# Performance work log

Measured on AMD Instinct MI355X. Metric: run time of the kernel, lower is better.

The kernel has to match this reference:

```python
import jax, jax.numpy as jnp
import numpy as np
from jax.scipy.special import gammaln, logsumexp

S, K, O, H = 64, 16, 32, 30   # state_dim, act_dim, obs_dim, horizon
T, N = 200, 512               # seq len, batch
EPS = 1e-6
LOG2PI = float(np.log(2.0 * np.pi))
NUM_PARAMS = S * O * 2 + K * S * S + S + S + 1


def setup_inputs() -> dict:
    key = jax.random.key(0)
    k1, k2, k3 = jax.random.split(key, 3)
    o = jax.random.normal(k1, (T, N, O), dtype=jnp.float32)
    a = jax.random.randint(k2, (T, N), 0, K)
    theta = jax.random.normal(k3, (N, NUM_PARAMS), dtype=jnp.float32)
    return {"o": o, "a": a, "theta": theta}


def _transform_params(theta):
    sizes = [S * O * 2, K * S * S, S, S, 1]
    idx = np.cumsum(sizes)[:-1]
    tA, tB, tC, tD, ttau = jnp.split(theta, idx, axis=-1)
    A_mean, A_lv = jnp.split(tA, 2, axis=-1)
    A_mean = A_mean.reshape(-1, S, O)
    A_std = jax.nn.softplus(A_lv.reshape(-1, S, O)) + EPS  # rectify
    B = jax.nn.softmax(tB.reshape(-1, K, S, S), axis=-1)
    C = jax.nn.softmax(tC.reshape(-1, 1, S), axis=-1)
    D = jax.nn.softmax(tD.reshape(-1, S), axis=-1)
    tau = jax.nn.sigmoid(ttau) * (2.0 * H) + 1.0  # [N,1]
    return A_mean, A_std, B, C, D, tau


def reference(o, a, theta):
    A_mean, A_std, B, C, D, tau = _transform_params(theta)

    # --- negative expected free energy reward: r[n,k,i] ---
    ent = jnp.sum(0.5 + 0.5 * LOG2PI + jnp.log(A_std), axis=-1)          # Normal entropy, [N,S]
    kl = jnp.sum(B * (jnp.log(B + EPS) - jnp.log(C[:, None] + EPS)), -1)  # KL(B || C), [N,K,S]
    eh = jnp.einsum('nkij,nj->nki', B, ent)
    r = -kl - eh

    # --- finite-horizon value iteration: q [H,N,K,S] ---
    def vi_step(qt, _):
        v = logsumexp(qt, axis=-2)                    # [N,S]
        qn = r + jnp.einsum('nkij,nj->nki', B, v)
        return qn, qn
    _, q_rest = jax.lax.scan(vi_step, r, None, length=H - 1)
    q = jnp.concatenate([r[None], q_rest], axis=0)

    # --- truncated poisson horizon weights: pdf [N,H] ---
    hh = jnp.arange(H, dtype=jnp.float32)
    logp_h = hh[None, :] * jnp.log(tau) - tau - gammaln(hh + 1.0)[None, :]
    pdf = jnp.exp(logp_h)
    pdf = pdf / jnp.sum(pdf, axis=-1, keepdims=True)

    batch_idx = jnp.arange(N)

    def time_step(b, inp):
        o_t, a_t = inp
        # policy from current belief
        qb = jnp.einsum('ni,hnki->hnk', b, q)
        pi_h = jax.nn.softmax(qb, axis=-1)
        pi_t = jnp.einsum('hnk,nh->nk', pi_h, pdf)
        # belief update
        B_a = B[batch_idx, a_t]                       # [N,S,S]
        s = jnp.einsum('nij,ni->nj', B_a, b)
        logp_s = jnp.log(s + EPS)
        lp = -0.5 * ((o_t[:, None, :] - A_mean) / A_std) ** 2 \
             - jnp.log(A_std) - 0.5 * LOG2PI          # [N,S,O]
        joint = logp_s + jnp.sum(lp, axis=-1)         # [N,S]
        b_next = jax.nn.softmax(joint, axis=-1)
        logp_o = logsumexp(joint, axis=-1)
        return b_next, (pi_t, b, logp_o)

    _, (pi, b_seq, logp_o) = jax.lax.scan(time_step, D, (o, a))
    return pi, b_seq, logp_o
```

## Files before the change

### kernel.cpp

```cpp
#include <hip/hip_runtime.h>
#include <hip/hip_bf16.h>
#include <math.h>

#define SDIM 64
#define KDIM 16
#define ODIM 32
#define HDIM 30
#define TDIM 200
#define NDIM 512
#define NP 69761
#define EPSV 1e-6f
#define LOG2PIF 1.8378770664093453f

__device__ __forceinline__ float softplusf(float x) {
    return (x > 0.f) ? x + log1pf(expf(-x)) : log1pf(expf(x));
}
__device__ __forceinline__ float wave_max64(float v) {
#pragma unroll
    for (int off = 32; off; off >>= 1) v = fmaxf(v, __shfl_xor(v, off, 64));
    return v;
}
__device__ __forceinline__ float wave_sum64(float v) {
#pragma unroll
    for (int off = 32; off; off >>= 1) v += __shfl_xor(v, off, 64);
// ... 7 lines not shown
    const float* __restrict__ theta, float* __restrict__ invstd,
    float* __restrict__ c0, float* __restrict__ ent,
    float* __restrict__ logC, float* __restrict__ Dws,
    float* __restrict__ pdfws)
{
    __shared__ float ls[SDIM * 33];
    const int n = blockIdx.x, tid = threadIdx.x;
    const float* thn = theta + (size_t)n * NP;

    for (int idx = tid; idx < SDIM * ODIM; idx += 256) {
        float x = thn[2048 + idx];
        float sp = softplusf(x) + EPSV;
        invstd[(size_t)n * SDIM * ODIM + idx] = 1.f / sp;
        int s = idx >> 5, oo = idx & 31;
        ls[s * 33 + oo] = logf(sp);
    }
    __syncthreads();

    const int wave = tid >> 6, lane = tid & 63;
    if (wave == 0) {
        float sum = 0.f;
#pragma unroll
        for (int oo = 0; oo < ODIM; ++oo) sum += ls[lane * 33 + oo];
        c0[n * SDIM + lane]  = -sum - 16.f * LOG2PIF;
        ent[n * SDIM + lane] =  sum + 32.f * (0.5f + 0.5f * LOG2PIF);
    } else if (wave == 1) {
        float x = thn[69632 + lane];
        float m = wave_max64(x);
        float e = expf(x - m);
        float ssum = wave_sum64(e);
        logC[n * SDIM + lane] = logf(e / ssum + EPSV);
    } else if (wave == 2) {
        float x = thn[69696 + lane];
        float m = wave_max64(x);
        float e = expf(x - m);
        float ssum = wave_sum64(e);
        Dws[n * SDIM + lane] = e / ssum;
    } else {
        float tt = thn[69760];
        float tau = 60.f / (1.f + expf(-tt)) + 1.f;
        float p = 0.f;
        if (lane < HDIM)
            p = expf((float)lane * logf(tau) - tau - lgammaf((float)lane + 1.f));
        float ssum = wave_sum64(p);
        if (lane < HDIM) pdfws[n * HDIM + lane] = p / ssum;
    }
}

__global__ __launch_bounds__(256) void row_stats_kernel(
    const float* __restrict__ theta, const float* __restrict__ logC,
    const float* __restrict__ ent, float* __restrict__ lse,
    float* __restrict__ rws, __hip_bfloat16* __restrict__ bn)
{
    const int gw = blockIdx.x * 4 + (threadIdx.x >> 6);
    const int lane = threadIdx.x & 63;
    const int n = gw >> 10, rl = gw & 1023;
    float x = theta[(size_t)n * NP + 4096 + (size_t)rl * 64 + lane];
    float m = wave_max64(x);
    float e = expf(x - m);
    float ssum = wave_sum64(e);
    float Bj = e / ssum;
    if (bn) {
        const int k = rl >> 6, i = rl & 63;
        __hip_bfloat16 h = __float2bfloat16(Bj);
        unsigned short bits;
        __builtin_memcpy(&bits, &h, 2);
        ((unsigned short*)bn)[(size_t)n * KDIM * SDIM * SDIM
            + (size_t)k * 4096 + (size_t)(i >> 1) * 128 + lane * 2 + (i & 1)] = bits;
    }
    float contrib = Bj * (logf(Bj + EPSV) - logC[n * SDIM + lane] + ent[n * SDIM + lane]);
    contrib = wave_sum64(contrib);
    if (lane == 0) {
        lse[gw] = m + logf(ssum);
        rws[gw] = -contrib;
    }
}

#define BS4(T_, U_) do {                                                       \
    const int cur_ = (T_) & 1, nxt_ = cur_ ^ 1;                                \
    if (wave == 3) out_b[((size_t)(T_) * NDIM + n) * SDIM + lane] = bval;      \
    {      \
        float a0_ = 0.f, a1_ = 0.f, a2_ = 0.f, a3_ = 0.f;                      \
        _Pragma("unroll")                                                      \
        for (int j_ = 0; j_ < 4; ++j_) {                                       \
            a0_ += er[4 * j_ + 0] * __shfl(bval, rbase + 4 * j_ + 0, 64);      \
            a1_ += er[4 * j_ + 1] * __shfl(bval, rbase + 4 * j_ + 1, 64);      \
            a2_ += er[4 * j_ + 2] * __shfl(bval, rbase + 4 * j_ + 2, 64);      \
            a3_ += er[4 * j_ + 3] * __shfl(bval, rbase + 4 * j_ + 3, 64);      \
        }                                                                      \
        part_s[cur_][wave][lane] = (a0_ + a1_) + (a2_ + a3_);                  \
    }                                                                          \
    if ((T_) + 1 < TDIM) {                             \
        const float* om_ = &o_s[((T_) + 1) * ODIM + ob];                       \
        float zz_ = 0.f;                                                       \
        _Pragma("unroll")                                                      \
        for (int j_ = 0; j_ < 8; ++j_) {                                       \
            float z_ = (om_[j_] - mean_r[j_]) * istd_r[j_];                    \
            zz_ += z_ * z_;                                                    \
        }                                                                      \
        z2p_s[nxt_][wave][lane] = zz_;                                         \
    }                                                                          \
    _Pragma("unroll")                             \
    for (int m_ = 0; m_ < 8; ++m_) {                                           \
        er[2 * m_]     = __uint_as_float(U_[m_] << 16);                        \
        er[2 * m_ + 1] = __uint_as_float(U_[m_] & 0xffff0000u);                \
    }                                                                          \
    {                                                 \
        const int tl_ = ((T_) + 3 < TDIM) ? (T_) + 3 : TDIM - 1;               \
        const uint* up_ = bnn32 + (size_t)a_s[tl_] * 2048 + (rbase >> 1) * 64 + lane; \
        _Pragma("unroll")                                                      \
        for (int m_ = 0; m_ < 8; ++m_) U_[m_] = up_[m_ * 64];                  \
    }                                                                          \
    bar_lds();                                            \
    {            \
        float sv_ = part_s[cur_][0][lane] + part_s[cur_][1][lane]              \
                  + part_s[cur_][2][lane] + part_s[cur_][3][lane];             \
        float u_ = (sv_ + EPSV) * ecz_cur;                                     \
        float S_ = wave_sum64(u_);                                             \
        if (wave == 0 && lane == 0)                                            \
            out_lp[(size_t)(T_) * NDIM + n] = cm_cur + __logf(S_);             \
        bval = u_ / S_;                                                        \
        float z2n_ = z2p_s[nxt_][0][lane] + z2p_s[nxt_][1][lane]               \
                   + z2p_s[nxt_][2][lane] + z2p_s[nxt_][3][lane];              \
        float cn_ = c0_r - 0.5f * z2n_;                                        \
        cm_cur = wave_max64(cn_);                                              \
        ecz_cur = __expf(cn_ - cm_cur);                                        \
    }                                                                          \
} while (0)

__global__ __launch_bounds__(256) void belief4_kernel(
    const float* __restrict__ o, const int* __restrict__ a,
    const float* __restrict__ theta, const __hip_bfloat16* __restrict__ bn,
    const float* __restrict__ invstd, const float* __restrict__ c0g,
    const float* __restrict__ Dws,
    float* __restrict__ out_b, float* __restrict__ out_lp)
{
    __shared__ float o_s[TDIM * ODIM];
    __shared__ int   a_s[TDIM];
    __shared__ float mean_s[SDIM * 33];
    __shared__ float istd_s[SDIM * 33];
    __shared__ float c0_sh[SDIM];
    __shared__ float part_s[2][4][68];
    __shared__ float z2p_s[2][4][SDIM];

    const int n = blockIdx.x, tid = threadIdx.x;
    const int wave = tid >> 6, lane = tid & 63;
    const int rbase = wave * 16, ob = wave * 8;
    const float* thn = theta + (size_t)n * NP;
    const uint* bnn32 = (const uint*)(bn + (size_t)n * KDIM * SDIM * SDIM);

    for (int idx = tid; idx < TDIM * ODIM; idx += 256)
        o_s[idx] = o[((size_t)(idx >> 5) * NDIM + n) * ODIM + (idx & 31)];
    if (tid < TDIM) a_s[tid] = a[tid * NDIM + n];
    for (int idx = tid; idx < SDIM * ODIM; idx += 256) {
        int s = idx >> 5, oo = idx & 31;
        mean_s[s * 33 + oo] = thn[idx];
        istd_s[s * 33 + oo] = invstd[(size_t)n * SDIM * ODIM + idx];
    }
    if (tid < SDIM) c0_sh[tid] = c0g[n * SDIM + tid];
    __syncthreads();

    const float c0_r = c0_sh[lane];
    float bval = Dws[n * SDIM + lane];
    float mean_r[8], istd_r[8];
#pragma unroll
    for (int j = 0; j < 8; ++j) {
        mean_r[j] = mean_s[lane * 33 + ob + j];
        istd_r[j] = istd_s[lane * 33 + ob + j];
    }

    float er[16];
    uint u0[8], u1[8];
    {
        const uint* p0 = bnn32 + (size_t)a_s[0] * 2048 + (rbase >> 1) * 64 + lane;
#pragma unroll
        for (int m = 0; m < 8; ++m) u0[m] = p0[m * 64];
#pragma unroll
        for (int m = 0; m < 8; ++m) {
            er[2 * m]     = __uint_as_float(u0[m] << 16);
            er[2 * m + 1] = __uint_as_float(u0[m] & 0xffff0000u);
        }
        const uint* p1 = bnn32 + (size_t)a_s[1] * 2048 + (rbase >> 1) * 64 + lane;
#pragma unroll
        for (int m = 0; m < 8; ++m) u0[m] = p1[m * 64];
        const uint* p2 = bnn32 + (size_t)a_s[2] * 2048 + (rbase >> 1) * 64 + lane;
#pragma unroll
        for (int m = 0; m < 8; ++m) u1[m] = p2[m * 64];
    }
    {
        const float* om = &o_s[ob];
        float zz = 0.f;
#pragma unroll
        for (int j = 0; j < 8; ++j) {
            float z = (om[j] - mean_r[j]) * istd_r[j];
            zz += z * z;
        }
        z2p_s[0][wave][lane] = zz;
    }
    __syncthreads();
    float ecz_cur, cm_cur;
    {
        float z2 = z2p_s[0][0][lane] + z2p_s[0][1][lane]
                 + z2p_s[0][2][lane] + z2p_s[0][3][lane];
        float c = c0_r - 0.5f * z2;
        cm_cur = wave_max64(c);
        ecz_cur = __expf(c - cm_cur);
    }

#pragma unroll 1
    for (int t = 0; t < TDIM; t += 2) {
        BS4(t, u0);
        BS4(t + 1, u1);
    }
}

#define Z2PART(TT_, BUF_) do {                                                 \
    const int ob_ = (wave - 1) * 8;                                            \
    const float* om_ = &o_s[(TT_) * ODIM + ob_];                               \
    float zz_ = 0.f;                                                           \
    _Pragma("unroll")                                                          \
    for (int j_ = 0; j_ < 8; ++j_) {                                           \
        float z_ = (om_[j_] - mean_s[lane * 33 + ob_ + j_])                    \
                 * istd_s[lane * 33 + ob_ + j_];                               \
        zz_ += z_ * z_;                                                        \
    }                                                                          \
    z2p_s[BUF_][wave - 1][lane] = zz_;                                         \
} while (0)

#define BSTEP(T_, RAW_) do {                                                   \
    const int cur_ = (T_) & 1, nxt_ = cur_ ^ 1;                                \
    if (wave >= 1) {                                                           \
        float acc_ = 0.f;                                                      \
        _Pragma("unroll")                                                      \
        for (int ii = 0; ii < 10; ++ii)                                        \
            if (ii < nrow) acc_ += er[ii] * b_s[cur_][rbase + ii];             \
        part_s[wave - 1][lane] = acc_;                                         \
        if (wave == 6) out_b[((size_t)(T_) * NDIM + n) * SDIM + lane] = b_s[cur_][lane]; \
    }                                                                          \
    bar_lds();                                                                 \
    if (wave == 0) {                                                           \
        float sv_ = part_s[0][lane] + part_s[1][lane] + part_s[2][lane]        \
                  + part_s[3][lane] + part_s[4][lane] + part_s[5][lane]        \
                  + part_s[6][lane];                                           \
        float z2_ = z2p_s[cur_][0][lane] + z2p_s[cur_][1][lane]                \
                  + z2p_s[cur_][2][lane] + z2p_s[cur_][3][lane];               \
        float joint_ = __logf(sv_ + EPSV) + c0_s[lane] - 0.5f * z2_;           \
        float m_ = wave_max64(joint_);                                         \
        float e_ = __expf(joint_ - m_);                                        \
        float ss_ = wave_sum64(e_);                                            \
        b_s[nxt_][lane] = e_ / ss_;                                            \
        if (lane == 0) out_lp[(size_t)(T_) * NDIM + n] = m_ + __logf(ss_);     \
    } else {                                                                   \
        if ((T_) + 1 < TDIM) {                                                 \
            const int an_ = a_s[(T_) + 1];                                     \
            const float* ln_ = lseA + an_ * SDIM;                              \
            _Pragma("unroll")                                                  \
            for (int ii = 0; ii < 10; ++ii)                                    \
                if (ii < nrow) er[ii] = __expf(RAW_[ii] - ln_[rbase + ii]);    \
            if (wave <= 4) Z2PART((T_) + 1, nxt_);                             \
        }                                                                      \
        const int tl_ = ((T_) + 3 < TDIM) ? (T_) + 3 : TDIM - 1;               \
        const int a3_ = a_s[tl_];                                              \
        const float* X3_ = Xn + (size_t)a3_ * SDIM * SDIM;                     \
        _Pragma("unroll")                                                      \
        for (int ii = 0; ii < 10; ++ii)                                        \
// ... 17 lines not shown
    __shared__ float c0_s[SDIM];
    __shared__ float b_s[2][SDIM];
    __shared__ float part_s[7][68];
    __shared__ float z2p_s[2][4][SDIM];

    const int n = blockIdx.x, tid = threadIdx.x;
    const int wave = tid >> 6, lane = tid & 63;
    const float* thn = theta + (size_t)n * NP;
    const float* Xn  = thn + 4096;

    for (int idx = tid; idx < TDIM * ODIM; idx += 512)
        o_s[idx] = o[((size_t)(idx >> 5) * NDIM + n) * ODIM + (idx & 31)];
    if (tid < TDIM) a_s[tid] = a[tid * NDIM + n];
    for (int idx = tid; idx < SDIM * ODIM; idx += 512) {
        int s = idx >> 5, oo = idx & 31;
        mean_s[s * 33 + oo] = thn[idx];
        istd_s[s * 33 + oo] = invstd[(size_t)n * SDIM * ODIM + idx];
    }
    for (int idx = tid; idx < KDIM * SDIM; idx += 512)
        lseA[idx] = lse[(size_t)n * KDIM * SDIM + idx];
    if (tid < SDIM) { c0_s[tid] = c0g[n * SDIM + tid]; b_s[0][tid] = Dws[n * SDIM + tid]; }
    __syncthreads();

    const int rbase = (wave >= 1) ? (wave - 1) * 10 : 0;
    const int nrow  = (wave >= 1) ? ((SDIM - rbase) < 10 ? (SDIM - rbase) : 10) : 0;

    float er[10], raw0[10], raw1[10];
    if (wave >= 1) {
        const int a0 = a_s[0];
        const float* X0 = Xn + (size_t)a0 * SDIM * SDIM;
        const float* l0 = lseA + a0 * SDIM;
#pragma unroll
        for (int ii = 0; ii < 10; ++ii)
            if (ii < nrow) er[ii] = __expf(X0[(size_t)(rbase + ii) * SDIM + lane] - l0[rbase + ii]);
        const int a1 = a_s[1];
        const float* X1 = Xn + (size_t)a1 * SDIM * SDIM;
#pragma unroll
        for (int ii = 0; ii < 10; ++ii)
            if (ii < nrow) raw0[ii] = X1[(size_t)(rbase + ii) * SDIM + lane];
        const int a2 = a_s[2];
        const float* X2 = Xn + (size_t)a2 * SDIM * SDIM;
#pragma unroll
        for (int ii = 0; ii < 10; ++ii)
            if (ii < nrow) raw1[ii] = X2[(size_t)(rbase + ii) * SDIM + lane];
        if (wave <= 4) Z2PART(0, 0);
    }
    __syncthreads();

#pragma unroll 1
    for (int t = 0; t < TDIM; t += 2) {
        BSTEP(t, raw0);
        BSTEP(t + 1, raw1);
    }
}

__global__ __launch_bounds__(512) void vi_kernel(
    const float* __restrict__ theta, const float* __restrict__ lse,
    const float* __restrict__ rws, float* __restrict__ q_ws)
{
    __shared__ float q_lds[KDIM * 68];
    __shared__ __align__(16) float v_lds[68];
    const int n = blockIdx.x, tid = threadIdx.x;
    const float* Xn = theta + (size_t)n * NP + 4096;

    const float l0  = lse[(size_t)n * 1024 + tid];
    const float l1  = lse[(size_t)n * 1024 + 512 + tid];
    const float rr0 = rws[(size_t)n * 1024 + tid];
    const float rr1 = rws[(size_t)n * 1024 + 512 + tid];

    float4 er0[16], er1[16];
    {
        const float* X0 = Xn + (size_t)tid * 64;
        const float* X1 = Xn + (size_t)(512 + tid) * 64;
#pragma unroll
        for (int j = 0; j < 16; ++j) {
            float4 x = *(const float4*)(X0 + j * 4);
            er0[j] = make_float4(__expf(x.x - l0), __expf(x.y - l0),
                                 __expf(x.z - l0), __expf(x.w - l0));
            float4 y = *(const float4*)(X1 + j * 4);
            er1[j] = make_float4(__expf(y.x - l1), __expf(y.y - l1),
                                 __expf(y.z - l1), __expf(y.w - l1));
        }
    }

    float qr0 = rr0, qr1 = rr1;
    float* qw = q_ws + (size_t)n * HDIM * 1024;
    const int kq0 = tid >> 6, iq = tid & 63;
    qw[tid] = qr0;
    qw[512 + tid] = qr1;
    q_lds[kq0 * 68 + iq] = qr0;
    q_lds[(8 + kq0) * 68 + iq] = qr1;
    __syncthreads();

#pragma unroll 1
    for (int h = 1; h < HDIM; ++h) {
        if (tid < 64) {
            float m = -1e30f;
#pragma unroll
            for (int k = 0; k < KDIM; ++k) m = fmaxf(m, q_lds[k * 68 + tid]);
            float s = 0.f;
#pragma unroll
            for (int k = 0; k < KDIM; ++k) s += __expf(q_lds[k * 68 + tid] - m);
            v_lds[tid] = m + __logf(s);
        }
        bar_lds();
        float a0x = 0.f, a0y = 0.f, a0z = 0.f, a0w = 0.f;
        float a1x = 0.f, a1y = 0.f, a1z = 0.f, a1w = 0.f;
#pragma unroll
        for (int jq = 0; jq < 16; ++jq) {
            const float4 v4 = *(const float4*)&v_lds[jq * 4];
            a0x += er0[jq].x * v4.x; a0y += er0[jq].y * v4.y;
            a0z += er0[jq].z * v4.z; a0w += er0[jq].w * v4.w;
            a1x += er1[jq].x * v4.x; a1y += er1[jq].y * v4.y;
            a1z += er1[jq].z * v4.z; a1w += er1[jq].w * v4.w;
        }
        qr0 = rr0 + ((a0x + a0y) + (a0z + a0w));
        qr1 = rr1 + ((a1x + a1y) + (a1z + a1w));
        qw[(size_t)h * 1024 + tid] = qr0;
        qw[(size_t)h * 1024 + 512 + tid] = qr1;
        q_lds[kq0 * 68 + iq] = qr0;
        q_lds[(8 + kq0) * 68 + iq] = qr1;
        bar_lds();
    }
}

__global__ __launch_bounds__(512, 1) void policy_bc_kernel(
    const float* __restrict__ q_ws, const float* __restrict__ out_b_g,
    const float* __restrict__ pdfg, float* __restrict__ out_pi)
{
    __shared__ __align__(16) float b_all[TDIM * SDIM];
    __shared__ float part[2][8][8][17];
    __shared__ float pdf_s[32];

    const int n = blockIdx.x, tid = threadIdx.x;
    const int w = tid >> 6, lane = tid & 63;
    const int hl = lane >> 4, kk = lane & 15;
    const int hown = w * 4 + hl;
    const float* qn = q_ws + (size_t)n * HDIM * 1024;

    for (int idx = tid; idx < TDIM * 16; idx += 512) {
        const int t = idx >> 4, jq = idx & 15;
        *(float4*)&b_all[t * SDIM + jq * 4] =
            *(const float4*)&out_b_g[((size_t)t * NDIM + n) * SDIM + jq * 4];
    }
    if (tid < 32) pdf_s[tid] = (tid < HDIM) ? pdfg[n * HDIM + tid] : 0.f;

    float4 qrow[16];
    if (hown < HDIM) {
#pragma unroll
        for (int jq = 0; jq < 16; ++jq)
            qrow[jq] = *(const float4*)&qn[(size_t)hown * 1024 + kk * 64 + jq * 4];
    } else {
#pragma unroll
        for (int jq = 0; jq < 16; ++jq)
            qrow[jq] = make_float4(0.f, 0.f, 0.f, 0.f);
    }
    __syncthreads();
    const float pdfh = pdf_s[hown];

#define PVAL(T_, OUTV_) do {                                                   \
    const float* br_ = &b_all[(T_) * SDIM];                                    \
    float ax_ = 0.f, ay_ = 0.f, az_ = 0.f, aw_ = 0.f;                          \
    _Pragma("unroll")                                                          \
    for (int jq_ = 0; jq_ < 16; ++jq_) {                                       \
        const float4 b4_ = *(const float4*)&br_[jq_ * 4];                      \
        ax_ += qrow[jq_].x * b4_.x; ay_ += qrow[jq_].y * b4_.y;                \
        az_ += qrow[jq_].z * b4_.z; aw_ += qrow[jq_].w * b4_.w;                \
    }                                                                          \
    float acc_ = (ax_ + ay_) + (az_ + aw_);                                    \
    float m_ = acc_;                                                           \
    m_ = fmaxf(m_, __shfl_xor(m_, 1, 64));                                     \
    m_ = fmaxf(m_, __shfl_xor(m_, 2, 64));                                     \
    m_ = fmaxf(m_, __shfl_xor(m_, 4, 64));                                     \
    m_ = fmaxf(m_, __shfl_xor(m_, 8, 64));                                     \
    float e_ = __expf(acc_ - m_);                                              \
    float S_ = e_;                                                             \
    S_ += __shfl_xor(S_, 1, 64);                                               \
    S_ += __shfl_xor(S_, 2, 64);                                               \
    S_ += __shfl_xor(S_, 4, 64);                                               \
    S_ += __shfl_xor(S_, 8, 64);                                               \
    float v_ = pdfh * e_ / S_;                                                 \
    v_ += __shfl_xor(v_, 16, 64);                                              \
    v_ += __shfl_xor(v_, 32, 64);                                              \
    OUTV_ = v_;                                                                \
} while (0)

#pragma unroll 1
    for (int t0 = 0; t0 < TDIM; t0 += 8) {
        const int buf = (t0 >> 3) & 1;
        float v0, v1, v2, v3, v4, v5, v6, v7;
        PVAL(t0 + 0, v0); PVAL(t0 + 1, v1); PVAL(t0 + 2, v2); PVAL(t0 + 3, v3);
        PVAL(t0 + 4, v4); PVAL(t0 + 5, v5); PVAL(t0 + 6, v6); PVAL(t0 + 7, v7);
        if (lane < 16) {
            part[buf][0][w][lane] = v0; part[buf][1][w][lane] = v1;
            part[buf][2][w][lane] = v2; part[buf][3][w][lane] = v3;
            part[buf][4][w][lane] = v4; part[buf][5][w][lane] = v5;
            part[buf][6][w][lane] = v6; part[buf][7][w][lane] = v7;
        }
        bar_lds();
        if (lane < 16) {
            float s8 = 0.f;
#pragma unroll
            for (int ww = 0; ww < 8; ++ww) s8 += part[buf][w][ww][lane];
            out_pi[((size_t)(t0 + w) * NDIM + n) * KDIM + lane] = s8;
        }
    }
#undef PVAL
}

__global__ __launch_bounds__(512) void vi_policy_kernel(
    const float* __restrict__ theta, const float* __restrict__ lse,
    const float* __restrict__ rws, const float* __restrict__ pdfg,
    const float* __restrict__ out_b_g, float* __restrict__ out_pi)
{
    __shared__ __align__(16) float q_s[HDIM * KDIM * 68];
    __shared__ float r_s[KDIM * SDIM];
    __shared__ float lse_s[KDIM * SDIM];
    __shared__ __align__(16) float v_s[SDIM];
    __shared__ __align__(16) float b_lds[64 * 68];
    __shared__ float pdf_s[32];

    const int n = blockIdx.x, tid = threadIdx.x;
    const int wave = tid >> 6, lane = tid & 63;
    const int sub = lane & 15, rq = lane >> 4;
    const float* Xn = theta + (size_t)n * NP + 4096;

    for (int idx = tid; idx < KDIM * SDIM; idx += 512) {
        r_s[idx]   = rws[(size_t)n * KDIM * SDIM + idx];
        lse_s[idx] = lse[(size_t)n * KDIM * SDIM + idx];
    }
    if (tid < HDIM) pdf_s[tid] = pdfg[n * HDIM + tid];
    __syncthreads();

    for (int idx = tid; idx < KDIM * SDIM; idx += 512)
        q_s[(idx >> 6) * 68 + (idx & 63)] = r_s[idx];

    float4 breg[32];
#pragma unroll
    for (int it = 0; it < 32; ++it) {
        const int row = it * 32 + wave * 4 + rq;
        const float* xr = Xn + (size_t)row * SDIM + sub * 4;
        const float l = lse_s[row];
        breg[it] = make_float4(__expf(xr[0] - l), __expf(xr[1] - l),
                               __expf(xr[2] - l), __expf(xr[3] - l));
    }
    bar_lds();

#pragma unroll 1
    for (int h = 1; h < HDIM; ++h) {
        if (tid < SDIM) {
            const int base = (h - 1) * KDIM;
            float m = -1e30f;
#pragma unroll
            for (int k = 0; k < KDIM; ++k) m = fmaxf(m, q_s[(base + k) * 68 + tid]);
            float ssum = 0.f;
#pragma unroll
            for (int k = 0; k < KDIM; ++k) ssum += __expf(q_s[(base + k) * 68 + tid] - m);
            v_s[tid] = m + __logf(ssum);
        }
        bar_lds();
// ... 53 lines not shown
            mA = fmaxf(mA, __shfl_xor(mA, 2, 64));
            mA = fmaxf(mA, __shfl_xor(mA, 4, 64));
            mA = fmaxf(mA, __shfl_xor(mA, 8, 64));
            mB = fmaxf(mB, __shfl_xor(mB, 1, 64));
            mB = fmaxf(mB, __shfl_xor(mB, 2, 64));
            mB = fmaxf(mB, __shfl_xor(mB, 4, 64));
            mB = fmaxf(mB, __shfl_xor(mB, 8, 64));
            float eA = __expf(aA - mA), eB = __expf(aB - mB);
            float SA = eA, SB = eB;
            SA += __shfl_xor(SA, 1, 64);
            SA += __shfl_xor(SA, 2, 64);
            SA += __shfl_xor(SA, 4, 64);
            SA += __shfl_xor(SA, 8, 64);
            SB += __shfl_xor(SB, 1, 64);
            SB += __shfl_xor(SB, 2, 64);
            SB += __shfl_xor(SB, 4, 64);
            SB += __shfl_xor(SB, 8, 64);
            const float ph = pdf_s[h];
            pikA += ph * eA / SA;
            pikB += ph * eB / SB;
        }
        if (vA) out_pi[(((size_t)(t0 + tc)) * NDIM + n) * KDIM + kk] = pikA;
        if (vB) out_pi[(((size_t)(t0 + 32 + tc)) * NDIM + n) * KDIM + kk] = pikB;
        bar_lds();
    }
}

extern "C" void kernel_launch(void* const* d_in, const int* in_sizes, int n_in,
                              void* d_out, int out_size, void* d_ws, size_t ws_size,
                              hipStream_t stream) {
    (void)in_sizes; (void)n_in; (void)out_size;
    const float* o     = (const float*)d_in[0];
    const int*   a     = (const int*)d_in[1];
    const float* theta = (const float*)d_in[2];
    float* out = (float*)d_out;
    float* ws  = (float*)d_ws;

    float* lse    = ws;
    float* rws    = lse    + (size_t)NDIM * KDIM * SDIM;
    float* invstd = rws    + (size_t)NDIM * KDIM * SDIM;
    float* c0     = invstd + (size_t)NDIM * SDIM * ODIM;
    float* ent    = c0     + (size_t)NDIM * SDIM;
    float* logC   = ent    + (size_t)NDIM * SDIM;
    float* Dws    = logC   + (size_t)NDIM * SDIM;
    float* pdfws  = Dws    + (size_t)NDIM * SDIM;
    float* q_ws   = pdfws  + (size_t)NDIM * HDIM;
    __hip_bfloat16* bn = (__hip_bfloat16*)(q_ws + (size_t)NDIM * HDIM * KDIM * SDIM);

    const size_t f_base = (size_t)NDIM * KDIM * SDIM * 2
                        + (size_t)NDIM * SDIM * ODIM
                        + (size_t)NDIM * SDIM * 4
                        + (size_t)NDIM * HDIM;
    const size_t f_q  = (size_t)NDIM * HDIM * KDIM * SDIM;
    const size_t need2 = (f_base + f_q) * 4;
    const size_t need1 = need2 + (size_t)NDIM * KDIM * SDIM * SDIM * 2;

    float* out_pi = out;
    float* out_b  = out + (size_t)TDIM * NDIM * KDIM;
    float* out_lp = out + (size_t)TDIM * NDIM * KDIM + (size_t)TDIM * NDIM * SDIM;

    transform_kernel<<<NDIM, 256, 0, stream>>>(theta, invstd, c0, ent, logC, Dws, pdfws);

    if (ws_size >= need1) {
        row_stats_kernel<<<(NDIM * KDIM * SDIM) / 4, 256, 0, stream>>>(
            theta, logC, ent, lse, rws, bn);
        belief4_kernel<<<NDIM, 256, 0, stream>>>(
            o, a, theta, bn, invstd, c0, Dws, out_b, out_lp);
        vi_kernel<<<NDIM, 512, 0, stream>>>(theta, lse, rws, q_ws);
        policy_bc_kernel<<<NDIM, 512, 0, stream>>>(q_ws, out_b, pdfws, out_pi);
    } else if (ws_size >= need2) {
        row_stats_kernel<<<(NDIM * KDIM * SDIM) / 4, 256, 0, stream>>>(
            theta, logC, ent, lse, rws, (__hip_bfloat16*)nullptr);
        belief_kernel<<<NDIM, 512, 0, stream>>>(
            o, a, theta, lse, invstd, c0, Dws, out_b, out_lp);
        vi_kernel<<<NDIM, 512, 0, stream>>>(theta, lse, rws, q_ws);
        policy_bc_kernel<<<NDIM, 512, 0, stream>>>(q_ws, out_b, pdfws, out_pi);
    } else {
        row_stats_kernel<<<(NDIM * KDIM * SDIM) / 4, 256, 0, stream>>>(
            theta, logC, ent, lse, rws, (__hip_bfloat16*)nullptr);
        belief_kernel<<<NDIM, 512, 0, stream>>>(
            o, a, theta, lse, invstd, c0, Dws, out_b, out_lp);
        vi_policy_kernel<<<NDIM, 512, 0, stream>>>(theta, lse, rws, pdfws, out_b, out_pi);
    }
}
```

Measured before the change: 643.4 us.

## Halve policy kernel threads with two horizons per lane and bf16 beliefs in LDS

The policy kernel now runs 256 threads, and each lane owns two horizon rows of q in registers instead of one, so every belief read from LDS is reused twice. The per-sequence belief buffer is stored in LDS as bf16 and unpacked with shifts and masks. This halves LDS use and read traffic, which could let more blocks fit per CU. The cost is lower precision in the belief-q dot product and about twice the register pressure per thread.

```diff
diff --git a/kernel.cpp b/kernel.cpp
--- a/kernel.cpp
+++ b/kernel.cpp
@@ -437,62 +437,92 @@
     }
 }
 
-__global__ __launch_bounds__(512, 1) void policy_bc_kernel(
+__global__ __launch_bounds__(256, 1) void policy_p2_kernel(
     const float* __restrict__ q_ws, const float* __restrict__ out_b_g,
     const float* __restrict__ pdfg, float* __restrict__ out_pi)
 {
-    __shared__ __align__(16) float b_all[TDIM * SDIM];
-    __shared__ float part[2][8][8][17];
+    __shared__ __align__(16) unsigned short b16[TDIM * SDIM];
+    __shared__ float part[2][8][4][17];
     __shared__ float pdf_s[32];
 
     const int n = blockIdx.x, tid = threadIdx.x;
     const int w = tid >> 6, lane = tid & 63;
     const int hl = lane >> 4, kk = lane & 15;
-    const int hown = w * 4 + hl;
+    const int h0 = w * 8 + hl, h1 = h0 + 4;
     const float* qn = q_ws + (size_t)n * HDIM * 1024;
 
-    for (int idx = tid; idx < TDIM * 16; idx += 512) {
-        const int t = idx >> 4, jq = idx & 15;
-        *(float4*)&b_all[t * SDIM + jq * 4] =
-            *(const float4*)&out_b_g[((size_t)t * NDIM + n) * SDIM + jq * 4];
+    for (int idx = tid; idx < TDIM * SDIM; idx += 256) {
+        float bv = out_b_g[((size_t)(idx >> 6) * NDIM + n) * SDIM + (idx & 63)];
+        __hip_bfloat16 hb = __float2bfloat16(bv);
+        unsigned short bits; __builtin_memcpy(&bits, &hb, 2);
+        b16[idx] = bits;
     }
     if (tid < 32) pdf_s[tid] = (tid < HDIM) ? pdfg[n * HDIM + tid] : 0.f;
 
-    float4 qrow[16];
-    if (hown < HDIM) {
+    float4 q0[16], q1[16];
+    if (h0 < HDIM) {
 #pragma unroll
         for (int jq = 0; jq < 16; ++jq)
-            qrow[jq] = *(const float4*)&qn[(size_t)hown * 1024 + kk * 64 + jq * 4];
+            q0[jq] = *(const float4*)&qn[(size_t)h0 * 1024 + kk * 64 + jq * 4];
     } else {
 #pragma unroll
+        for (int jq = 0; jq < 16; ++jq) q0[jq] = make_float4(0.f, 0.f, 0.f, 0.f);
+    }
+    if (h1 < HDIM) {
+#pragma unroll
         for (int jq = 0; jq < 16; ++jq)
-            qrow[jq] = make_float4(0.f, 0.f, 0.f, 0.f);
+            q1[jq] = *(const float4*)&qn[(size_t)h1 * 1024 + kk * 64 + jq * 4];
+    } else {
+#pragma unroll
+        for (int jq = 0; jq < 16; ++jq) q1[jq] = make_float4(0.f, 0.f, 0.f, 0.f);
     }
     __syncthreads();
-    const float pdfh = pdf_s[hown];
-
-#define PVAL(T_, OUTV_) do {                                                   \
-    const float* br_ = &b_all[(T_) * SDIM];                                    \
-    float ax_ = 0.f, ay_ = 0.f, az_ = 0.f, aw_ = 0.f;                          \
+    const float pdf0 = pdf_s[h0], pdf1 = pdf_s[h1];
+
+#define PVAL2(T_, OUTV_) do {                                                  \
+    const uint4* bp_ = (const uint4*)&b16[(T_) * SDIM];                        \
+    float a0x_ = 0.f, a0y_ = 0.f, a0z_ = 0.f, a0w_ = 0.f;                      \
+    float a1x_ = 0.f, a1y_ = 0.f, a1z_ = 0.f, a1w_ = 0.f;                      \
     _Pragma("unroll")                                                          \
-    for (int jq_ = 0; jq_ < 16; ++jq_) {                                       \
-        const float4 b4_ = *(const float4*)&br_[jq_ * 4];                      \
-        ax_ += qrow[jq_].x * b4_.x; ay_ += qrow[jq_].y * b4_.y;                \
-        az_ += qrow[jq_].z * b4_.z; aw_ += qrow[jq_].w * b4_.w;                \
-    }                                                                          \
-    float acc_ = (ax_ + ay_) + (az_ + aw_);                                    \
-    float m_ = acc_;                                                           \
-    m_ = fmaxf(m_, __shfl_xor(m_, 1, 64));                                     \
-    m_ = fmaxf(m_, __shfl_xor(m_, 2, 64));                                     \
-    m_ = fmaxf(m_, __shfl_xor(m_, 4, 64));                                     \
-    m_ = fmaxf(m_, __shfl_xor(m_, 8, 64));                                     \
-    float e_ = __expf(acc_ - m_);                                              \
-    float S_ = e_;                                                             \
-    S_ += __shfl_xor(S_, 1, 64);                                               \
-    S_ += __shfl_xor(S_, 2, 64);                                               \
-    S_ += __shfl_xor(S_, 4, 64);                                               \
-    S_ += __shfl_xor(S_, 8, 64);                                               \
-    float v_ = pdfh * e_ / S_;                                                 \
+    for (int r_ = 0; r_ < 8; ++r_) {                                           \
+        const uint4 u_ = bp_[r_];                                              \
+        const float b0_ = __uint_as_float(u_.x << 16);                         \
+        const float b1_ = __uint_as_float(u_.x & 0xffff0000u);                 \
+        const float b2_ = __uint_as_float(u_.y << 16);                         \
+        const float b3_ = __uint_as_float(u_.y & 0xffff0000u);                 \
+        const float b4_ = __uint_as_float(u_.z << 16);                         \
+        const float b5_ = __uint_as_float(u_.z & 0xffff0000u);                 \
+        const float b6_ = __uint_as_float(u_.w << 16);                         \
+        const float b7_ = __uint_as_float(u_.w & 0xffff0000u);                 \
+        const float4 qa0_ = q0[2 * r_], qb0_ = q0[2 * r_ + 1];                 \
+        const float4 qa1_ = q1[2 * r_], qb1_ = q1[2 * r_ + 1];                 \
+        a0x_ += qa0_.x * b0_; a0y_ += qa0_.y * b1_;                            \
+        a0z_ += qa0_.z * b2_; a0w_ += qa0_.w * b3_;                            \
+        a0x_ += qb0_.x * b4_; a0y_ += qb0_.y * b5_;                            \
+        a0z_ += qb0_.z * b6_; a0w_ += qb0_.w * b7_;                            \
+        a1x_ += qa1_.x * b0_; a1y_ += qa1_.y * b1_;                            \
+        a1z_ += qa1_.z * b2_; a1w_ += qa1_.w * b3_;                            \
+        a1x_ += qb1_.x * b4_; a1y_ += qb1_.y * b5_;                            \
+        a1z_ += qb1_.z * b6_; a1w_ += qb1_.w * b7_;                            \
+    }                                                                          \
+    float acc0_ = (a0x_ + a0y_) + (a0z_ + a0w_);                               \
+    float acc1_ = (a1x_ + a1y_) + (a1z_ + a1w_);                               \
+    float m0_ = acc0_, m1_ = acc1_;                                            \
+    m0_ = fmaxf(m0_, __shfl_xor(m0_, 1, 64));                                  \
+    m1_ = fmaxf(m1_, __shfl_xor(m1_, 1, 64));                                  \
+    m0_ = fmaxf(m0_, __shfl_xor(m0_, 2, 64));                                  \
+    m1_ = fmaxf(m1_, __shfl_xor(m1_, 2, 64));                                  \
+    m0_ = fmaxf(m0_, __shfl_xor(m0_, 4, 64));                                  \
+    m1_ = fmaxf(m1_, __shfl_xor(m1_, 4, 64));                                  \
+    m0_ = fmaxf(m0_, __shfl_xor(m0_, 8, 64));                                  \
+    m1_ = fmaxf(m1_, __shfl_xor(m1_, 8, 64));                                  \
+    float e0_ = __expf(acc0_ - m0_), e1_ = __expf(acc1_ - m1_);                \
+    float S0_ = e0_, S1_ = e1_;                                                \
+    S0_ += __shfl_xor(S0_, 1, 64);  S1_ += __shfl_xor(S1_, 1, 64);             \
+    S0_ += __shfl_xor(S0_, 2, 64);  S1_ += __shfl_xor(S1_, 2, 64);             \
+    S0_ += __shfl_xor(S0_, 4, 64);  S1_ += __shfl_xor(S1_, 4, 64);             \
+    S0_ += __shfl_xor(S0_, 8, 64);  S1_ += __shfl_xor(S1_, 8, 64);             \
+    float v_ = pdf0 * e0_ / S0_ + pdf1 * e1_ / S1_;                            \
     v_ += __shfl_xor(v_, 16, 64);                                              \
     v_ += __shfl_xor(v_, 32, 64);                                              \
     OUTV_ = v_;                                                                \
@@ -502,8 +532,8 @@
     for (int t0 = 0; t0 < TDIM; t0 += 8) {
         const int buf = (t0 >> 3) & 1;
         float v0, v1, v2, v3, v4, v5, v6, v7;
-        PVAL(t0 + 0, v0); PVAL(t0 + 1, v1); PVAL(t0 + 2, v2); PVAL(t0 + 3, v3);
-        PVAL(t0 + 4, v4); PVAL(t0 + 5, v5); PVAL(t0 + 6, v6); PVAL(t0 + 7, v7);
+        PVAL2(t0 + 0, v0); PVAL2(t0 + 1, v1); PVAL2(t0 + 2, v2); PVAL2(t0 + 3, v3);
+        PVAL2(t0 + 4, v4); PVAL2(t0 + 5, v5); PVAL2(t0 + 6, v6); PVAL2(t0 + 7, v7);
         if (lane < 16) {
             part[buf][0][w][lane] = v0; part[buf][1][w][lane] = v1;
             part[buf][2][w][lane] = v2; part[buf][3][w][lane] = v3;
@@ -512,13 +542,15 @@
         }
         bar_lds();
         if (lane < 16) {
-            float s8 = 0.f;
-#pragma unroll
-            for (int ww = 0; ww < 8; ++ww) s8 += part[buf][w][ww][lane];
-            out_pi[((size_t)(t0 + w) * NDIM + n) * KDIM + lane] = s8;
-        }
-    }
-#undef PVAL
+            float sA = part[buf][w][0][lane] + part[buf][w][1][lane]
+                     + part[buf][w][2][lane] + part[buf][w][3][lane];
+            out_pi[((size_t)(t0 + w) * NDIM + n) * KDIM + lane] = sA;
+            float sB = part[buf][w + 4][0][lane] + part[buf][w + 4][1][lane]
+                     + part[buf][w + 4][2][lane] + part[buf][w + 4][3][lane];
+            out_pi[((size_t)(t0 + 4 + w) * NDIM + n) * KDIM + lane] = sB;
+        }
+    }
+#undef PVAL2
 }
 
 __global__ __launch_bounds__(512) void vi_policy_kernel(
@@ -693,14 +725,14 @@
         belief4_kernel<<<NDIM, 256, 0, stream>>>(
             o, a, theta, bn, invstd, c0, Dws, out_b, out_lp);
         vi_kernel<<<NDIM, 512, 0, stream>>>(theta, lse, rws, q_ws);
-        policy_bc_kernel<<<NDIM, 512, 0, stream>>>(q_ws, out_b, pdfws, out_pi);
+        policy_p2_kernel<<<NDIM, 256, 0, stream>>>(q_ws, out_b, pdfws, out_pi);
     } else if (ws_size >= need2) {
         row_stats_kernel<<<(NDIM * KDIM * SDIM) / 4, 256, 0, stream>>>(
             theta, logC, ent, lse, rws, (__hip_bfloat16*)nullptr);
         belief_kernel<<<NDIM, 512, 0, stream>>>(
             o, a, theta, lse, invstd, c0, Dws, out_b, out_lp);
         vi_kernel<<<NDIM, 512, 0, stream>>>(theta, lse, rws, q_ws);
-        policy_bc_kernel<<<NDIM, 512, 0, stream>>>(q_ws, out_b, pdfws, out_pi);
+        policy_p2_kernel<<<NDIM, 256, 0, stream>>>(q_ws, out_b, pdfws, out_pi);
     } else {
         row_stats_kernel<<<(NDIM * KDIM * SDIM) / 4, 256, 0, stream>>>(
             theta, logC, ent, lse, rws, (__hip_bfloat16*)nullptr);
```

Result: slower. 661.0 us (+2.7%).

## Fuse policy computation into belief recurrence and batch row-stats rows per wave

Applied to the files above, without the earlier changes.

The separate policy kernel is removed. Its per-timestep q·b softmax and pdf-weighted mix now run inside the belief recurrence, using q rows held in registers and the current belief shared through LDS. This drops the re-read of the belief sequence from global memory and one kernel launch, but it lengthens every serial belief step and raises register pressure (launch bounds 256,2). The row-stats kernel now handles 16 rows per wave with fewer blocks, and vi_kernel must run before the fused kernel.

```diff
diff --git a/kernel.cpp b/kernel.cpp
--- a/kernel.cpp
+++ b/kernel.cpp
@@ -83,34 +83,114 @@
     const float* __restrict__ ent, float* __restrict__ lse,
     float* __restrict__ rws, __hip_bfloat16* __restrict__ bn)
 {
-    const int gw = blockIdx.x * 4 + (threadIdx.x >> 6);
     const int lane = threadIdx.x & 63;
-    const int n = gw >> 10, rl = gw & 1023;
-    float x = theta[(size_t)n * NP + 4096 + (size_t)rl * 64 + lane];
-    float m = wave_max64(x);
-    float e = expf(x - m);
-    float ssum = wave_sum64(e);
-    float Bj = e / ssum;
-    if (bn) {
-        const int k = rl >> 6, i = rl & 63;
-        __hip_bfloat16 h = __float2bfloat16(Bj);
-        unsigned short bits;
-        __builtin_memcpy(&bits, &h, 2);
-        ((unsigned short*)bn)[(size_t)n * KDIM * SDIM * SDIM
-            + (size_t)k * 4096 + (size_t)(i >> 1) * 128 + lane * 2 + (i & 1)] = bits;
-    }
-    float contrib = Bj * (logf(Bj + EPSV) - logC[n * SDIM + lane] + ent[n * SDIM + lane]);
-    contrib = wave_sum64(contrib);
-    if (lane == 0) {
-        lse[gw] = m + logf(ssum);
-        rws[gw] = -contrib;
-    }
-}
-
-#define BS4(T_, U_) do {                                                       \
+    const int base_row = (blockIdx.x * 4 + (threadIdx.x >> 6)) * 16;
+    const int n = base_row >> 10;
+    const float lC = logC[n * SDIM + lane];
+    const float en = ent[n * SDIM + lane];
+    const float* thb = theta + (size_t)n * NP + 4096;
+    unsigned short* bns = bn ? (unsigned short*)bn + (size_t)n * KDIM * SDIM * SDIM : nullptr;
+
+#pragma unroll 1
+    for (int r = 0; r < 16; ++r) {
+        const int row = base_row + r;
+        const int rl = row & 1023;
+        float x = thb[(size_t)rl * 64 + lane];
+        float m = wave_max64(x);
+        float e = expf(x - m);
+        float ssum = wave_sum64(e);
+        float Bj = e / ssum;
+        if (bns) {
+            const int k = rl >> 6, i = rl & 63;
+            __hip_bfloat16 h = __float2bfloat16(Bj);
+            unsigned short bits;
+            __builtin_memcpy(&bits, &h, 2);
+            bns[(size_t)k * 4096 + (size_t)(i >> 1) * 128 + lane * 2 + (i & 1)] = bits;
+        }
+        float contrib = Bj * (logf(Bj + EPSV) - lC + en);
+        contrib = wave_sum64(contrib);
+        if (lane == 0) {
+            lse[row] = m + logf(ssum);
+            rws[row] = -contrib;
+        }
+    }
+}
+
+__global__ __launch_bounds__(512) void vi_kernel(
+    const float* __restrict__ theta, const float* __restrict__ lse,
+    const float* __restrict__ rws, float* __restrict__ q_ws)
+{
+    __shared__ float q_lds[KDIM * 68];
+    __shared__ __align__(16) float v_lds[68];
+    const int n = blockIdx.x, tid = threadIdx.x;
+    const float* Xn = theta + (size_t)n * NP + 4096;
+
+    const float l0  = lse[(size_t)n * 1024 + tid];
+    const float l1  = lse[(size_t)n * 1024 + 512 + tid];
+    const float rr0 = rws[(size_t)n * 1024 + tid];
+    const float rr1 = rws[(size_t)n * 1024 + 512 + tid];
+
+    float4 er0[16], er1[16];
+    {
+        const float* X0 = Xn + (size_t)tid * 64;
+        const float* X1 = Xn + (size_t)(512 + tid) * 64;
+#pragma unroll
+        for (int j = 0; j < 16; ++j) {
+            float4 x = *(const float4*)(X0 + j * 4);
+            er0[j] = make_float4(__expf(x.x - l0), __expf(x.y - l0),
+                                 __expf(x.z - l0), __expf(x.w - l0));
+            float4 y = *(const float4*)(X1 + j * 4);
+            er1[j] = make_float4(__expf(y.x - l1), __expf(y.y - l1),
+                                 __expf(y.z - l1), __expf(y.w - l1));
+        }
+    }
+
+    float qr0 = rr0, qr1 = rr1;
+    float* qw = q_ws + (size_t)n * HDIM * 1024;
+    const int kq0 = tid >> 6, iq = tid & 63;
+    qw[tid] = qr0;
+    qw[512 + tid] = qr1;
+    q_lds[kq0 * 68 + iq] = qr0;
+    q_lds[(8 + kq0) * 68 + iq] = qr1;
+    __syncthreads();
+
+#pragma unroll 1
+    for (int h = 1; h < HDIM; ++h) {
+        if (tid < 64) {
+            float m = -1e30f;
+#pragma unroll
+            for (int k = 0; k < KDIM; ++k) m = fmaxf(m, q_lds[k * 68 + tid]);
+            float s = 0.f;
+#pragma unroll
+            for (int k = 0; k < KDIM; ++k) s += __expf(q_lds[k * 68 + tid] - m);
+            v_lds[tid] = m + __logf(s);
+        }
+        bar_lds();
+        float a0x = 0.f, a0y = 0.f, a0z = 0.f, a0w = 0.f;
+        float a1x = 0.f, a1y = 0.f, a1z = 0.f, a1w = 0.f;
+#pragma unroll
+        for (int jq = 0; jq < 16; ++jq) {
+            const float4 v4 = *(const float4*)&v_lds[jq * 4];
+            a0x += er0[jq].x * v4.x; a0y += er0[jq].y * v4.y;
+            a0z += er0[jq].z * v4.z; a0w += er0[jq].w * v4.w;
+            a1x += er1[jq].x * v4.x; a1y += er1[jq].y * v4.y;
+            a1z += er1[jq].z * v4.z; a1w += er1[jq].w * v4.w;
+        }
+        qr0 = rr0 + ((a0x + a0y) + (a0z + a0w));
+        qr1 = rr1 + ((a1x + a1y) + (a1z + a1w));
+        qw[(size_t)h * 1024 + tid] = qr0;
+        qw[(size_t)h * 1024 + 512 + tid] = qr1;
+        q_lds[kq0 * 68 + iq] = qr0;
+        q_lds[(8 + kq0) * 68 + iq] = qr1;
+        bar_lds();
+    }
+}
+
+#define BSP(T_, U_) do {                                                       \
     const int cur_ = (T_) & 1, nxt_ = cur_ ^ 1;                                \
     if (wave == 3) out_b[((size_t)(T_) * NDIM + n) * SDIM + lane] = bval;      \
-    {      \
+    if (wave == 1) b2_s[cur_][lane] = bval;                                    \
+    {                                       \
         float a0_ = 0.f, a1_ = 0.f, a2_ = 0.f, a3_ = 0.f;                      \
         _Pragma("unroll")                                                      \
         for (int j_ = 0; j_ < 4; ++j_) {                                       \
@@ -143,7 +223,7 @@
         for (int m_ = 0; m_ < 8; ++m_) U_[m_] = up_[m_ * 64];                  \
     }                                                                          \
     bar_lds();                                            \
-    {            \
+    {                   \
         float sv_ = part_s[cur_][0][lane] + part_s[cur_][1][lane]              \
                   + part_s[cur_][2][lane] + part_s[cur_][3][lane];             \
         float u_ = (sv_ + EPSV) * ecz_cur;                                     \
@@ -157,14 +237,54 @@
         cm_cur = wave_max64(cn_);                                              \
         ecz_cur = __expf(cn_ - cm_cur);                                        \
     }                                                                          \
+    {                     \
+        float aAx_ = 0.f, aAy_ = 0.f, aAz_ = 0.f, aAw_ = 0.f;                  \
+        float aBx_ = 0.f, aBy_ = 0.f, aBz_ = 0.f, aBw_ = 0.f;                  \
+        _Pragma("unroll")                                                      \
+        for (int jq_ = 0; jq_ < 16; ++jq_) {                                   \
+            const float4 b4_ = *(const float4*)&b2_s[cur_][jq_ * 4];           \
+            aAx_ += qA[jq_].x * b4_.x; aAy_ += qA[jq_].y * b4_.y;              \
+            aAz_ += qA[jq_].z * b4_.z; aAw_ += qA[jq_].w * b4_.w;              \
+            aBx_ += qB[jq_].x * b4_.x; aBy_ += qB[jq_].y * b4_.y;              \
+            aBz_ += qB[jq_].z * b4_.z; aBw_ += qB[jq_].w * b4_.w;              \
+        }                                                                      \
+        float aA_ = (aAx_ + aAy_) + (aAz_ + aAw_);                             \
+        float aB_ = (aBx_ + aBy_) + (aBz_ + aBw_);                             \
+        float mA_ = aA_, mB_ = aB_;                                            \
+        mA_ = fmaxf(mA_, __shfl_xor(mA_, 1, 64));                              \
+        mB_ = fmaxf(mB_, __shfl_xor(mB_, 1, 64));                              \
+        mA_ = fmaxf(mA_, __shfl_xor(mA_, 2, 64));                              \
+        mB_ = fmaxf(mB_, __shfl_xor(mB_, 2, 64));                              \
+        mA_ = fmaxf(mA_, __shfl_xor(mA_, 4, 64));                              \
+        mB_ = fmaxf(mB_, __shfl_xor(mB_, 4, 64));                              \
+        mA_ = fmaxf(mA_, __shfl_xor(mA_, 8, 64));                              \
+        mB_ = fmaxf(mB_, __shfl_xor(mB_, 8, 64));                              \
+        float eA_ = __expf(aA_ - mA_), eB_ = __expf(aB_ - mB_);                \
+        float SA_ = eA_, SB_ = eB_;                                            \
+        SA_ += __shfl_xor(SA_, 1, 64);  SB_ += __shfl_xor(SB_, 1, 64);         \
+        SA_ += __shfl_xor(SA_, 2, 64);  SB_ += __shfl_xor(SB_, 2, 64);         \
+        SA_ += __shfl_xor(SA_, 4, 64);  SB_ += __shfl_xor(SB_, 4, 64);         \
+        SA_ += __shfl_xor(SA_, 8, 64);  SB_ += __shfl_xor(SB_, 8, 64);         \
+        float val_ = pdfA * eA_ / SA_ + pdfB * eB_ / SB_;                      \
+        val_ += __shfl_xor(val_, 16, 64);                                      \
+        val_ += __shfl_xor(val_, 32, 64);                                      \
+        if (lane < 16) p2_s[cur_][wave][lane] = val_;                          \
+        if ((T_) > 0 && wave == 3 && lane < 16) {                              \
+            float s4_ = p2_s[nxt_][0][lane] + p2_s[nxt_][1][lane]              \
+                      + p2_s[nxt_][2][lane] + p2_s[nxt_][3][lane];             \
+            out_pi[((size_t)((T_) - 1) * NDIM + n) * KDIM + lane] = s4_;       \
+        }                                                                      \
+    }                                                                          \
 } while (0)
 
-__global__ __launch_bounds__(256) void belief4_kernel(
+__global__ __launch_bounds__(256, 2) void bp_kernel(
     const float* __restrict__ o, const int* __restrict__ a,
     const float* __restrict__ theta, const __hip_bfloat16* __restrict__ bn,
     const float* __restrict__ invstd, const float* __restrict__ c0g,
-    const float* __restrict__ Dws,
-    float* __restrict__ out_b, float* __restrict__ out_lp)
+    const float* __restrict__ Dws, const float* __restrict__ pdfg,
+    const float* __restrict__ q_ws,
+    float* __restrict__ out_pi, float* __restrict__ out_b,
+    float* __restrict__ out_lp)
 {
     __shared__ float o_s[TDIM * ODIM];
     __shared__ int   a_s[TDIM];
@@ -173,6 +293,8 @@
     __shared__ float c0_sh[SDIM];
     __shared__ float part_s[2][4][68];
     __shared__ float z2p_s[2][4][SDIM];
+    __shared__ __align__(16) float b2_s[2][SDIM];
+    __shared__ float p2_s[2][4][17];
 
     const int n = blockIdx.x, tid = threadIdx.x;
     const int wave = tid >> 6, lane = tid & 63;
@@ -189,6 +311,23 @@
         istd_s[s * 33 + oo] = invstd[(size_t)n * SDIM * ODIM + idx];
     }
     if (tid < SDIM) c0_sh[tid] = c0g[n * SDIM + tid];
+
+    const int hA = tid >> 4, kA = tid & 15, hB = hA + 16;
+    const float* qnp = q_ws + (size_t)n * HDIM * 1024;
+    float4 qA[16], qB[16];
+#pragma unroll
+    for (int jq = 0; jq < 16; ++jq)
+        qA[jq] = *(const float4*)&qnp[(size_t)hA * 1024 + kA * 64 + jq * 4];
+    if (hB < HDIM) {
+#pragma unroll
+        for (int jq = 0; jq < 16; ++jq)
+            qB[jq] = *(const float4*)&qnp[(size_t)hB * 1024 + kA * 64 + jq * 4];
+    } else {
+#pragma unroll
+        for (int jq = 0; jq < 16; ++jq) qB[jq] = make_float4(0.f, 0.f, 0.f, 0.f);
+    }
+    const float pdfA = pdfg[n * HDIM + hA];
+    const float pdfB = (hB < HDIM) ? pdfg[n * HDIM + hB] : 0.f;
     __syncthreads();
 
     const float c0_r = c0_sh[lane];
@@ -240,8 +379,14 @@
 
 #pragma unroll 1
     for (int t = 0; t < TDIM; t += 2) {
-        BS4(t, u0);
-        BS4(t + 1, u1);
+        BSP(t, u0);
+        BSP(t + 1, u1);
+    }
+    __syncthreads();
+    if (wave == 3 && lane < 16) {
+        float s4 = p2_s[1][0][lane] + p2_s[1][1][lane]
+                 + p2_s[1][2][lane] + p2_s[1][3][lane];
+        out_pi[((size_t)(TDIM - 1) * NDIM + n) * KDIM + lane] = s4;
     }
 }
 
@@ -365,160 +510,6 @@
         BSTEP(t, raw0);
         BSTEP(t + 1, raw1);
     }
-}
-
-__global__ __launch_bounds__(512) void vi_kernel(
-    const float* __restrict__ theta, const float* __restrict__ lse,
-    const float* __restrict__ rws, float* __restrict__ q_ws)
-{
-    __shared__ float q_lds[KDIM * 68];
-    __shared__ __align__(16) float v_lds[68];
-    const int n = blockIdx.x, tid = threadIdx.x;
-    const float* Xn = theta + (size_t)n * NP + 4096;
-
-    const float l0  = lse[(size_t)n * 1024 + tid];
-    const float l1  = lse[(size_t)n * 1024 + 512 + tid];
-    const float rr0 = rws[(size_t)n * 1024 + tid];
-    const float rr1 = rws[(size_t)n * 1024 + 512 + tid];
-
-    float4 er0[16], er1[16];
-    {
-        const float* X0 = Xn + (size_t)tid * 64;
-        const float* X1 = Xn + (size_t)(512 + tid) * 64;
-#pragma unroll
-        for (int j = 0; j < 16; ++j) {
-            float4 x = *(const float4*)(X0 + j * 4);
-            er0[j] = make_float4(__expf(x.x - l0), __expf(x.y - l0),
-                                 __expf(x.z - l0), __expf(x.w - l0));
-            float4 y = *(const float4*)(X1 + j * 4);
-            er1[j] = make_float4(__expf(y.x - l1), __expf(y.y - l1),
-                                 __expf(y.z - l1), __expf(y.w - l1));
-        }
-    }
-
-    float qr0 = rr0, qr1 = rr1;
-    float* qw = q_ws + (size_t)n * HDIM * 1024;
-    const int kq0 = tid >> 6, iq = tid & 63;
-    qw[tid] = qr0;
-    qw[512 + tid] = qr1;
-    q_lds[kq0 * 68 + iq] = qr0;
-    q_lds[(8 + kq0) * 68 + iq] = qr1;
-    __syncthreads();
-
-#pragma unroll 1
-    for (int h = 1; h < HDIM; ++h) {
-        if (tid < 64) {
-            float m = -1e30f;
-#pragma unroll
-            for (int k = 0; k < KDIM; ++k) m = fmaxf(m, q_lds[k * 68 + tid]);
-            float s = 0.f;
-#pragma unroll
-            for (int k = 0; k < KDIM; ++k) s += __expf(q_lds[k * 68 + tid] - m);
-            v_lds[tid] = m + __logf(s);
-        }
-        bar_lds();
-        float a0x = 0.f, a0y = 0.f, a0z = 0.f, a0w = 0.f;
-        float a1x = 0.f, a1y = 0.f, a1z = 0.f, a1w = 0.f;
-#pragma unroll
-        for (int jq = 0; jq < 16; ++jq) {
-            const float4 v4 = *(const float4*)&v_lds[jq * 4];
-            a0x += er0[jq].x * v4.x; a0y += er0[jq].y * v4.y;
-            a0z += er0[jq].z * v4.z; a0w += er0[jq].w * v4.w;
-            a1x += er1[jq].x * v4.x; a1y += er1[jq].y * v4.y;
-            a1z += er1[jq].z * v4.z; a1w += er1[jq].w * v4.w;
-        }
-        qr0 = rr0 + ((a0x + a0y) + (a0z + a0w));
-        qr1 = rr1 + ((a1x + a1y) + (a1z + a1w));
-        qw[(size_t)h * 1024 + tid] = qr0;
-        qw[(size_t)h * 1024 + 512 + tid] = qr1;
-        q_lds[kq0 * 68 + iq] = qr0;
-        q_lds[(8 + kq0) * 68 + iq] = qr1;
-        bar_lds();
-    }
-}
-
-__global__ __launch_bounds__(512, 1) void policy_bc_kernel(
-    const float* __restrict__ q_ws, const float* __restrict__ out_b_g,
-    const float* __restrict__ pdfg, float* __restrict__ out_pi)
-{
-    __shared__ __align__(16) float b_all[TDIM * SDIM];
-    __shared__ float part[2][8][8][17];
-    __shared__ float pdf_s[32];
-
-    const int n = blockIdx.x, tid = threadIdx.x;
-    const int w = tid >> 6, lane = tid & 63;
-    const int hl = lane >> 4, kk = lane & 15;
-    const int hown = w * 4 + hl;
-    const float* qn = q_ws + (size_t)n * HDIM * 1024;
-
-    for (int idx = tid; idx < TDIM * 16; idx += 512) {
-        const int t = idx >> 4, jq = idx & 15;
-        *(float4*)&b_all[t * SDIM + jq * 4] =
-            *(const float4*)&out_b_g[((size_t)t * NDIM + n) * SDIM + jq * 4];
-    }
-    if (tid < 32) pdf_s[tid] = (tid < HDIM) ? pdfg[n * HDIM + tid] : 0.f;
-
-    float4 qrow[16];
-    if (hown < HDIM) {
-#pragma unroll
-        for (int jq = 0; jq < 16; ++jq)
-            qrow[jq] = *(const float4*)&qn[(size_t)hown * 1024 + kk * 64 + jq * 4];
-    } else {
-#pragma unroll
-        for (int jq = 0; jq < 16; ++jq)
-            qrow[jq] = make_float4(0.f, 0.f, 0.f, 0.f);
-    }
-    __syncthreads();
-    const float pdfh = pdf_s[hown];
-
-#define PVAL(T_, OUTV_) do {                                                   \
-    const float* br_ = &b_all[(T_) * SDIM];                                    \
-    float ax_ = 0.f, ay_ = 0.f, az_ = 0.f, aw_ = 0.f;                          \
-    _Pragma("unroll")                                                          \
-    for (int jq_ = 0; jq_ < 16; ++jq_) {                                       \
-        const float4 b4_ = *(const float4*)&br_[jq_ * 4];                      \
-        ax_ += qrow[jq_].x * b4_.x; ay_ += qrow[jq_].y * b4_.y;                \
-        az_ += qrow[jq_].z * b4_.z; aw_ += qrow[jq_].w * b4_.w;                \
-    }                                                                          \
-    float acc_ = (ax_ + ay_) + (az_ + aw_);                                    \
-    float m_ = acc_;                                                           \
-    m_ = fmaxf(m_, __shfl_xor(m_, 1, 64));                                     \
-    m_ = fmaxf(m_, __shfl_xor(m_, 2, 64));                                     \
-    m_ = fmaxf(m_, __shfl_xor(m_, 4, 64));                                     \
-    m_ = fmaxf(m_, __shfl_xor(m_, 8, 64));                                     \
-    float e_ = __expf(acc_ - m_);                                              \
-    float S_ = e_;                                                             \
-    S_ += __shfl_xor(S_, 1, 64);                                               \
-    S_ += __shfl_xor(S_, 2, 64);                                               \
-    S_ += __shfl_xor(S_, 4, 64);                                               \
-    S_ += __shfl_xor(S_, 8, 64);                                               \
-    float v_ = pdfh * e_ / S_;                                                 \
-    v_ += __shfl_xor(v_, 16, 64);                                              \
-    v_ += __shfl_xor(v_, 32, 64);                                              \
-    OUTV_ = v_;                                                                \
-} while (0)
-
-#pragma unroll 1
-    for (int t0 = 0; t0 < TDIM; t0 += 8) {
-        const int buf = (t0 >> 3) & 1;
-        float v0, v1, v2, v3, v4, v5, v6, v7;
-        PVAL(t0 + 0, v0); PVAL(t0 + 1, v1); PVAL(t0 + 2, v2); PVAL(t0 + 3, v3);
-        PVAL(t0 + 4, v4); PVAL(t0 + 5, v5); PVAL(t0 + 6, v6); PVAL(t0 + 7, v7);
-        if (lane < 16) {
-            part[buf][0][w][lane] = v0; part[buf][1][w][lane] = v1;
-            part[buf][2][w][lane] = v2; part[buf][3][w][lane] = v3;
-            part[buf][4][w][lane] = v4; part[buf][5][w][lane] = v5;
-            part[buf][6][w][lane] = v6; part[buf][7][w][lane] = v7;
-        }
-        bar_lds();
-        if (lane < 16) {
-            float s8 = 0.f;
-#pragma unroll
-            for (int ww = 0; ww < 8; ++ww) s8 += part[buf][w][ww][lane];
-            out_pi[((size_t)(t0 + w) * NDIM + n) * KDIM + lane] = s8;
-        }
-    }
-#undef PVAL
 }
 
 __global__ __launch_bounds__(512) void vi_policy_kernel(
@@ -678,8 +669,8 @@
                         + (size_t)NDIM * SDIM * 4
                         + (size_t)NDIM * HDIM;
     const size_t f_q  = (size_t)NDIM * HDIM * KDIM * SDIM;
-    const size_t need2 = (f_base + f_q) * 4;
-    const size_t need1 = need2 + (size_t)NDIM * KDIM * SDIM * SDIM * 2;
+    const size_t need1 = (f_base + f_q) * 4
+                       + (size_t)NDIM * KDIM * SDIM * SDIM * 2;
 
     float* out_pi = out;
     float* out_b  = out + (size_t)TDIM * NDIM * KDIM;
@@ -688,21 +679,12 @@
     transform_kernel<<<NDIM, 256, 0, stream>>>(theta, invstd, c0, ent, logC, Dws, pdfws);
 
     if (ws_size >= need1) {
-        row_stats_kernel<<<(NDIM * KDIM * SDIM) / 4, 256, 0, stream>>>(
-            theta, logC, ent, lse, rws, bn);
-        belief4_kernel<<<NDIM, 256, 0, stream>>>(
-            o, a, theta, bn, invstd, c0, Dws, out_b, out_lp);
+        row_stats_kernel<<<8192, 256, 0, stream>>>(theta, logC, ent, lse, rws, bn);
         vi_kernel<<<NDIM, 512, 0, stream>>>(theta, lse, rws, q_ws);
-        policy_bc_kernel<<<NDIM, 512, 0, stream>>>(q_ws, out_b, pdfws, out_pi);
-    } else if (ws_size >= need2) {
-        row_stats_kernel<<<(NDIM * KDIM * SDIM) / 4, 256, 0, stream>>>(
-            theta, logC, ent, lse, rws, (__hip_bfloat16*)nullptr);
-        belief_kernel<<<NDIM, 512, 0, stream>>>(
-            o, a, theta, lse, invstd, c0, Dws, out_b, out_lp);
-        vi_kernel<<<NDIM, 512, 0, stream>>>(theta, lse, rws, q_ws);
-        policy_bc_kernel<<<NDIM, 512, 0, stream>>>(q_ws, out_b, pdfws, out_pi);
+        bp_kernel<<<NDIM, 256, 0, stream>>>(
+            o, a, theta, bn, invstd, c0, Dws, pdfws, q_ws, out_pi, out_b, out_lp);
     } else {
-        row_stats_kernel<<<(NDIM * KDIM * SDIM) / 4, 256, 0, stream>>>(
+        row_stats_kernel<<<8192, 256, 0, stream>>>(
             theta, logC, ent, lse, rws, (__hip_bfloat16*)nullptr);
         belief_kernel<<<NDIM, 512, 0, stream>>>(
             o, a, theta, lse, invstd, c0, Dws, out_b, out_lp);
```

Result: faster. 590.1 us, median of 2 (-8.3%).
